# Performance work log

Measured on AMD Instinct MI355X. Metric: run time of the kernel, lower is better.

The kernel has to match this reference:

```python
import jax, jax.numpy as jnp
import numpy as np

N_NODES = 50000
N_REL = 8
N_EDGES = 100000
IN_SIZE = 128
OUT_SIZE = 128


def setup_inputs() -> dict:
    key = jax.random.key(0)
    k1, k2, k3, k4, k5 = jax.random.split(key, 5)
    inp = jax.random.normal(k1, (N_NODES, IN_SIZE), dtype=jnp.float32)
    src = jax.random.randint(k2, (N_REL, N_EDGES), 0, N_NODES, dtype=jnp.int32)
    dst = jax.random.randint(k3, (N_REL, N_EDGES), 0, N_NODES, dtype=jnp.int32)
    vals = jax.random.uniform(k4, (N_REL, N_EDGES), dtype=jnp.float32)
    weights = jax.random.normal(k5, (N_REL, IN_SIZE, OUT_SIZE), dtype=jnp.float32) * (1.0 / np.sqrt(IN_SIZE))
    return {"inp": inp, "src": src, "dst": dst, "vals": vals, "weights": weights}


def reference(inp, src, dst, vals, weights):
    # Per-relation sparse adj @ inp:  agg[r] = A_r @ inp, A_r given as COO edges.
    n_nodes = inp.shape[0]

    def rel_agg(s, d, v):
        msgs = v[:, None] * inp[s]                      # [E, in]
        return jax.ops.segment_sum(msgs, d, num_segments=n_nodes)  # [N, in]

    agg = jax.vmap(rel_agg)(src, dst, vals)             # [R, N, in]
    # concat along features then block-stacked weight matmul == per-relation
    # matmul summed over relations: out = sum_r agg[r] @ W[r]
    out = jnp.einsum('rni,rio->no', agg, weights)       # [N, out]
    return out
```

## Files before the change

kernel.cpp:

```cpp
#include <hip/hip_runtime.h>


constexpr int IN  = 128;
constexpr int OUT = 128;
constexpr int LDK = 136;
constexpr int NPB = 64;
constexpr int LDKB = 136;
constexpr int CAPMAX = 256;
constexpr int NBINS_MAX = 1024;
constexpr int EPB = 1024;

typedef __attribute__((ext_vector_type(8))) short bf16x8;
typedef __attribute__((ext_vector_type(4))) float f32x4;

__device__ inline unsigned short f2bf(float f) {
    unsigned int u = __float_as_uint(f);
    u += 0x7fffu + ((u >> 16) & 1u);
    return (unsigned short)(u >> 16);
}
__device__ inline float bflo(unsigned int u) { return __uint_as_float(u << 16); }
__device__ inline float bfhi(unsigned int u) { return __uint_as_float(u & 0xffff0000u); }
__device__ inline unsigned int pack2bf(float a, float b) {
    return (unsigned)f2bf(a) | ((unsigned)f2bf(b) << 16);
}
__device__ inline unsigned int cvtpk_bf16(float a, float b) {
    unsigned int r;
    asm("v_cvt_pk_bf16_f32 %0, %1, %2" : "=v"(r) : "v"(a), "v"(b));
    return r;
}

__global__ __launch_bounds__(256) void conv_inp_kernel(
    const float* __restrict__ x, unsigned short* __restrict__ y, int n8)
{
    const int i = blockIdx.x * 256 + threadIdx.x;
    if (i >= n8) return;
    const float4 a = ((const float4*)x)[i * 2];
    const float4 b = ((const float4*)x)[i * 2 + 1];
    uint4 o;
    o.x = pack2bf(a.x, a.y);
    o.y = pack2bf(a.z, a.w);
    o.z = pack2bf(b.x, b.y);
    o.w = pack2bf(b.z, b.w);
    ((uint4*)y)[i] = o;
}

__global__ __launch_bounds__(256) void conv_w_kernel(
    const float* __restrict__ w, unsigned short* __restrict__ wt, int total)
{
    const int t = blockIdx.x * 256 + threadIdx.x;
    if (t >= total) return;
    const int r = t >> 14, rem = t & 16383;
    const int n = rem >> 7, k = rem & 127;
    wt[t] = f2bf(w[(r << 14) + (k << 7) + n]);
}

__global__ __launch_bounds__(256) void prep_kernel(
    const int* __restrict__ src, const int* __restrict__ dst,
    const float* __restrict__ vals, int* __restrict__ bin_cnt,
    int2* __restrict__ binned, int4* __restrict__ spill,
    int* __restrict__ spill_cnt,
    int n_edges, int n_nodes, int nbins, int cap, int spill_max,
    int fgx, int nF,
    const float* __restrict__ x, unsigned short* __restrict__ y, int n8, int nbI,
    const float* __restrict__ w, unsigned short* __restrict__ wtb, int wtot)
{
    __shared__ int hist[NBINS_MAX];
    __shared__ int gbase[NBINS_MAX];

    const int bid = blockIdx.x;
    const int tid = threadIdx.x;

    if (bid >= nF) {
        const int cb = bid - nF;
        if (cb < nbI) {
            const int i = cb * 256 + tid;
            if (i >= n8) return;
            const float4 a = ((const float4*)x)[i * 2];
            const float4 b = ((const float4*)x)[i * 2 + 1];
            uint4 o;
            o.x = pack2bf(a.x, a.y);
            o.y = pack2bf(a.z, a.w);
            o.z = pack2bf(b.x, b.y);
            o.w = pack2bf(b.z, b.w);
            ((uint4*)y)[i] = o;
        } else {
            const int t = (cb - nbI) * 256 + tid;
            if (t >= wtot) return;
            const int r = t >> 14, rem = t & 16383;
            const int n = rem >> 7, k = rem & 127;
            wtb[t] = f2bf(w[(r << 14) + (k << 7) + n]);
        }
        return;
    }

    const int rel = bid / fgx;
    const int e0 = (bid - rel * fgx) * EPB;
    const size_t base_e = (size_t)rel * n_edges;

    for (int b = tid; b < nbins; b += 256) hist[b] = 0;
    __syncthreads();

    #pragma unroll
    for (int j = 0; j < EPB / 256; ++j) {
        const int e = e0 + j * 256 + tid;
        if (e < n_edges) atomicAdd(&hist[dst[base_e + e] >> 6], 1);
    }
    __syncthreads();

    for (int b = tid; b < nbins; b += 256) {
        const int c = hist[b];
        gbase[b] = c ? atomicAdd(&bin_cnt[rel * nbins + b], c) : 0;
        hist[b] = 0;
    }
    __syncthreads();

    #pragma unroll
    for (int j = 0; j < EPB / 256; ++j) {
        const int e = e0 + j * 256 + tid;
        if (e >= n_edges) continue;
        const int d = dst[base_e + e];
        const int s = src[base_e + e];
        const float v = vals[base_e + e];
        const int b = d >> 6;
        const int lp = atomicAdd(&hist[b], 1);
        const int pos = gbase[b] + lp;
        if (pos < cap) {
            binned[(size_t)(rel * nbins + b) * cap + pos] =
                make_int2(((d & 63) << 19) | s, __float_as_int(v));
        } else {
            const int sp = atomicAdd(spill_cnt, 1);
            if (sp < spill_max)
                spill[sp] = make_int4(d, (rel << 19) | s, __float_as_int(v), 0);
        }
    }
}

__global__ __launch_bounds__(256, 4) void bin_gemm_kernel(
    const unsigned short* __restrict__ inpb,
    const unsigned short* __restrict__ wt,
    const int2* __restrict__ binned, const int* __restrict__ bin_cnt,
    float* __restrict__ out, int n_nodes, int nbins, int cap, int n_rel)
{
    __shared__ unsigned short Ab[NPB * LDKB];
    __shared__ int2 sorted[CAPMAX];
    __shared__ int lcnt[NPB];
    __shared__ int loff[NPB + 1];
    __shared__ int lcur[NPB];
    __shared__ int relcnt[8];

    const int bin = blockIdx.x;
    const int tid = threadIdx.x;
    const int wave = tid >> 6, lane = tid & 63;
    const int m = lane & 15, q = lane >> 4;

    if (tid < n_rel) {
        int c = bin_cnt[tid * nbins + bin];
        relcnt[tid] = c > cap ? cap : c;
    }
    if (tid < NPB) { lcnt[tid] = 0; lcur[tid] = 0; }
    __syncthreads();

    int2 ecur = make_int2((NPB - 1) << 19, 0);
    if (tid < relcnt[0])
        ecur = binned[(size_t)bin * cap + tid];

    f32x4 acc[4][2];
    #pragma unroll
    for (int mt = 0; mt < 4; ++mt) {
        acc[mt][0] = (f32x4){0.f, 0.f, 0.f, 0.f};
        acc[mt][1] = (f32x4){0.f, 0.f, 0.f, 0.f};
    }

    for (int r = 0; r < n_rel; ++r) {
        const int cnt = relcnt[r];

        const unsigned short* wtr = wt + ((size_t)r * OUT + wave * 32) * IN;
        bf16x8 bfrag[2][4];
        #pragma unroll
        for (int nt = 0; nt < 2; ++nt)
            #pragma unroll
            for (int ks = 0; ks < 4; ++ks)
                bfrag[nt][ks] = *(const bf16x8*)(
                    wtr + (size_t)(nt * 16 + m) * IN + ks * 32 + q * 8);

        {
            uint4* A4 = (uint4*)Ab;
            #pragma unroll
            for (int j = 0; j < (NPB * LDKB / 8 + 255) / 256; ++j) {
                const int idx = j * 256 + tid;
                if (idx < NPB * LDKB / 8)
                    A4[idx] = make_uint4(0u, 0u, 0u, 0u);
            }
        }
        if (tid < cnt) atomicAdd(&lcnt[(ecur.x >> 19) & (NPB - 1)], 1);
        __syncthreads();

        if (tid < NPB) {
            const int v = lcnt[tid];
            int incl = v;
            #pragma unroll
            for (int off = 1; off < NPB; off <<= 1) {
                const int t = __shfl_up(incl, off, NPB);
                if (tid >= off) incl += t;
            }
            loff[tid] = incl - v;
            if (tid == NPB - 1) loff[NPB] = incl;
        }
        __syncthreads();

        if (tid < cnt) {
            const int g = (ecur.x >> 19) & (NPB - 1);
            const int pos = atomicAdd(&lcur[g], 1);
            sorted[loff[g] + pos] = ecur;
        }
        if (tid < NPB) lcnt[tid] = 0;
        __syncthreads();

        int2 enext = make_int2((NPB - 1) << 19, 0);
        if (r + 1 < n_rel && tid < relcnt[r + 1])
            enext = binned[(size_t)((r + 1) * nbins + bin) * cap + tid];

        {
            const int g0 = wave * 16;
            const int gend = g0 + 15;
            const int start = loff[g0];
            const int end = loff[g0 + 16];
            int cur = g0;
            float a0 = 0.f, a1 = 0.f;
            for (int i = start; i < end; i += 8) {
                int2 e[8]; unsigned int u[8];
                #pragma unroll
                for (int k = 0; k < 8; ++k) {
                    const int idx = i + k;
                    e[k] = (idx < end) ? sorted[idx]
                                       : make_int2(gend << 19, 0);
                }
                #pragma unroll
                for (int k = 0; k < 8; ++k)
                    u[k] = ((const unsigned int*)(
                        inpb + (size_t)(e[k].x & 0x7ffff) * IN))[lane];
                #pragma unroll
                for (int k = 0; k < 8; ++k) {
                    const int ln = (e[k].x >> 19) & 63;
                    if (ln != cur) {
                        *(unsigned int*)&Ab[cur * LDKB + lane * 2] =
                            cvtpk_bf16(a0, a1);
                        a0 = 0.f; a1 = 0.f; cur = ln;
                    }
                    const float v = __int_as_float(e[k].y);
                    a0 += v * bflo(u[k]); a1 += v * bfhi(u[k]);
                }
            }
            *(unsigned int*)&Ab[cur * LDKB + lane * 2] = cvtpk_bf16(a0, a1);
        }
        if (tid < NPB) lcur[tid] = 0;
        __syncthreads();

        #pragma unroll
        for (int ks = 0; ks < 4; ++ks) {
            bf16x8 a[4];
            #pragma unroll
            for (int mt = 0; mt < 4; ++mt)
                a[mt] = *(const bf16x8*)&Ab[(mt * 16 + m) * LDKB
                                            + ks * 32 + q * 8];
            #pragma unroll
            for (int mt = 0; mt < 4; ++mt) {
                acc[mt][0] = __builtin_amdgcn_mfma_f32_16x16x32_bf16(
                    a[mt], bfrag[0][ks], acc[mt][0], 0, 0, 0);
                acc[mt][1] = __builtin_amdgcn_mfma_f32_16x16x32_bf16(
                    a[mt], bfrag[1][ks], acc[mt][1], 0, 0, 0);
            }
        }
        ecur = enext;
        __syncthreads();
    }

    const int row0 = bin * NPB;
    #pragma unroll
    for (int mt = 0; mt < 4; ++mt) {
        #pragma unroll
        for (int rg = 0; rg < 4; ++rg) {
            const int row = row0 + mt * 16 + q * 4 + rg;
            if (row < n_nodes) {
                float* op = out + (size_t)row * OUT + wave * 32 + m;
                op[0]  = acc[mt][0][rg];
                op[16] = acc[mt][1][rg];
            }
        }
    }
}

__global__ __launch_bounds__(256) void spill_w_kernel(
    const unsigned short* __restrict__ inpb,
    const unsigned short* __restrict__ wt,
    const int4* __restrict__ spill, const int* __restrict__ spill_cnt,
    float* __restrict__ out, int spill_max)
{
    int n = *spill_cnt;
    if (n > spill_max) n = spill_max;
    const int w = (blockIdx.x * 256 + threadIdx.x) >> 6;
    const int lane = threadIdx.x & 63;
    const int nw = gridDim.x * 4;
    for (int i = w; i < n; i += nw) {
        const int4 s = spill[i];
        const int d = s.x;
        const int rel = s.y >> 19, srcrow = s.y & 0x7ffff;
        const float v = __int_as_float(s.z);
        const unsigned short* irow = inpb + (size_t)srcrow * IN;
        #pragma unroll
        for (int cc = 0; cc < 2; ++cc) {
            const int col = lane * 2 + cc;
            const unsigned short* wrow = wt + ((size_t)rel * OUT + col) * IN;
            float acc = 0.f;
            for (int k8 = 0; k8 < IN; k8 += 8) {
                const uint4 iw = *(const uint4*)(irow + k8);
                const uint4 ww = *(const uint4*)(wrow + k8);
                acc += bflo(iw.x)*bflo(ww.x) + bfhi(iw.x)*bfhi(ww.x)
                     + bflo(iw.y)*bflo(ww.y) + bfhi(iw.y)*bfhi(ww.y)
                     + bflo(iw.z)*bflo(ww.z) + bfhi(iw.z)*bfhi(ww.z)
                     + bflo(iw.w)*bflo(ww.w) + bfhi(iw.w)*bfhi(ww.w);
            }
            __hip_atomic_fetch_add(out + (size_t)d * OUT + col, v * acc,
                                   __ATOMIC_RELAXED, __HIP_MEMORY_SCOPE_AGENT);
        }
    }
}

__global__ __launch_bounds__(256) void mfma_gemm(
    const unsigned short* __restrict__ inpb,
    const unsigned short* __restrict__ wt,
    unsigned short* __restrict__ h, int rel_base, int n_nodes)
{
    __shared__ unsigned short As[128 * LDK];

    const int rel = rel_base + blockIdx.y;
    const int row0 = blockIdx.x * 128;
    const int tid = threadIdx.x;
    const int wave = tid >> 6, lane = tid & 63;
    const int m = lane & 15, q = lane >> 4;

    {
        const int r = tid >> 1;
        const int half = (tid & 1) * 64;
        const int grow = row0 + r;
        const uint4* gp = (const uint4*)(inpb + (size_t)grow * IN + half);
        uint4* lp = (uint4*)&As[r * LDK + half];
        #pragma unroll
        for (int i = 0; i < 8; ++i) {
            uint4 v = make_uint4(0u, 0u, 0u, 0u);
            if (grow < n_nodes) v = gp[i];
            lp[i] = v;
        }
    }

    bf16x8 bfrag[2][4];
    {
        const unsigned short* wtr = wt + ((size_t)rel * OUT + wave * 32) * IN;
        #pragma unroll
        for (int nt = 0; nt < 2; ++nt)
            #pragma unroll
            for (int ks = 0; ks < 4; ++ks)
                bfrag[nt][ks] = *(const bf16x8*)(
                    wtr + (size_t)(nt * 16 + m) * IN + ks * 32 + q * 8);
    }

    __syncthreads();

    f32x4 acc[8][2];
    #pragma unroll
    for (int mt = 0; mt < 8; ++mt)
        #pragma unroll
        for (int nt = 0; nt < 2; ++nt)
            acc[mt][nt] = (f32x4){0.f, 0.f, 0.f, 0.f};

    #pragma unroll
    for (int ks = 0; ks < 4; ++ks) {
        bf16x8 a[8];
        #pragma unroll
        for (int mt = 0; mt < 8; ++mt)
            a[mt] = *(const bf16x8*)&As[(mt * 16 + m) * LDK + ks * 32 + q * 8];
        #pragma unroll
        for (int mt = 0; mt < 8; ++mt) {
            acc[mt][0] = __builtin_amdgcn_mfma_f32_16x16x32_bf16(
                a[mt], bfrag[0][ks], acc[mt][0], 0, 0, 0);
            acc[mt][1] = __builtin_amdgcn_mfma_f32_16x16x32_bf16(
                a[mt], bfrag[1][ks], acc[mt][1], 0, 0, 0);
        }
    }

    unsigned short* hrel = h + (size_t)blockIdx.y * n_nodes * OUT;
    #pragma unroll
    for (int mt = 0; mt < 8; ++mt) {
        #pragma unroll
        for (int rg = 0; rg < 4; ++rg) {
            const int row = row0 + mt * 16 + q * 4 + rg;
            if (row < n_nodes) {
                unsigned short* hp = hrel + (size_t)row * OUT + wave * 32 + m;
                hp[0]  = f2bf(acc[mt][0][rg]);
                hp[16] = f2bf(acc[mt][1][rg]);
            }
        }
    }
}

__global__ __launch_bounds__(256) void fill_kernel(
    const int* __restrict__ src, const int* __restrict__ dst,
    const float* __restrict__ vals, int* __restrict__ counts,
    int2* __restrict__ bucket, int4* __restrict__ spill,
    int* __restrict__ spill_cnt, int n_edges, int n_nodes,
    int cap, int spill_max)
{
    const int e = blockIdx.x * 256 + threadIdx.x;
    if (e >= n_edges) return;
    const size_t g = (size_t)blockIdx.y * n_edges + e;
    const int d = dst[g];
    const int enc = blockIdx.y * n_nodes + src[g];
    const int pos = atomicAdd(&counts[d], 1);
    if (pos < cap) {
        bucket[(size_t)d * cap + pos] = make_int2(enc, __float_as_int(vals[g]));
    } else {
        const int sp = atomicAdd(spill_cnt, 1);
        if (sp < spill_max)
            spill[sp] = make_int4(d, enc, __float_as_int(vals[g]), 0);
    }
}

__global__ __launch_bounds__(256) void gather_kernel(
    const unsigned short* __restrict__ h, const int2* __restrict__ bucket,
    const int* __restrict__ counts, float* __restrict__ out,
    int n_nodes, int cap, int accum)
{
    const int node = blockIdx.x * 8 + (threadIdx.x >> 5);
    const int lane = threadIdx.x & 31;
    if (node >= n_nodes) return;
    int cnt = counts[node];
    if (cnt > cap) cnt = cap;
    const int2* __restrict__ b = bucket + (size_t)node * cap;
    float4* __restrict__ op = (float4*)(out + (size_t)node * OUT);

    float4 acc = accum ? op[lane] : make_float4(0.f, 0.f, 0.f, 0.f);
    int j = 0;
    for (; j + 4 <= cnt; j += 4) {
        const int2 r0 = b[j], r1 = b[j + 1], r2 = b[j + 2], r3 = b[j + 3];
        const uint2 h0 = ((const uint2*)(h + (size_t)r0.x * OUT))[lane];
        const uint2 h1 = ((const uint2*)(h + (size_t)r1.x * OUT))[lane];
        const uint2 h2 = ((const uint2*)(h + (size_t)r2.x * OUT))[lane];
        const uint2 h3 = ((const uint2*)(h + (size_t)r3.x * OUT))[lane];
        const float v0 = __int_as_float(r0.y), v1 = __int_as_float(r1.y);
        const float v2 = __int_as_float(r2.y), v3 = __int_as_float(r3.y);
        acc.x += v0*bflo(h0.x) + v1*bflo(h1.x) + v2*bflo(h2.x) + v3*bflo(h3.x);
        acc.y += v0*bfhi(h0.x) + v1*bfhi(h1.x) + v2*bfhi(h2.x) + v3*bfhi(h3.x);
        acc.z += v0*bflo(h0.y) + v1*bflo(h1.y) + v2*bflo(h2.y) + v3*bflo(h3.y);
        acc.w += v0*bfhi(h0.y) + v1*bfhi(h1.y) + v2*bfhi(h2.y) + v3*bfhi(h3.y);
    }
    for (; j < cnt; ++j) {
        const int2 r0 = b[j];
        const float v = __int_as_float(r0.y);
        const uint2 hv = ((const uint2*)(h + (size_t)r0.x * OUT))[lane];
        acc.x += v * bflo(hv.x); acc.y += v * bfhi(hv.x);
        acc.z += v * bflo(hv.y); acc.w += v * bfhi(hv.y);
    }
    op[lane] = acc;
}

__global__ __launch_bounds__(256) void spill_kernel(
    const unsigned short* __restrict__ h, const int4* __restrict__ spill,
    const int* __restrict__ spill_cnt, float* __restrict__ out, int spill_max)
{
    int n = *spill_cnt;
    if (n > spill_max) n = spill_max;
    const int w = (blockIdx.x * 256 + threadIdx.x) >> 6;
    const int lane = threadIdx.x & 63;
    const int nw = gridDim.x * 4;
    for (int i = w; i < n; i += nw) {
        const int4 s = spill[i];
        const float v = __int_as_float(s.z);
        const unsigned int u = ((const unsigned int*)(h + (size_t)s.y * OUT))[lane];
        float* __restrict__ orow = out + (size_t)s.x * OUT;
        __hip_atomic_fetch_add(orow + lane * 2,     v * bflo(u),
                               __ATOMIC_RELAXED, __HIP_MEMORY_SCOPE_AGENT);
        __hip_atomic_fetch_add(orow + lane * 2 + 1, v * bfhi(u),
                               __ATOMIC_RELAXED, __HIP_MEMORY_SCOPE_AGENT);
    }
}

__global__ __launch_bounds__(256) void scatter_kernel(
    const unsigned short* __restrict__ h, const int* __restrict__ src,
    const int* __restrict__ dst, const float* __restrict__ vals,
    float* __restrict__ out, int n_edges)
{
    const int e = blockIdx.x * 8 + (threadIdx.x >> 5);
    if (e >= n_edges) return;
    const int lane = threadIdx.x & 31;
    const int s = src[e];
    const int d = dst[e];
    const float v = vals[e];
    const unsigned int* __restrict__ hrow =
        (const unsigned int*)(h + (size_t)s * OUT);
    float* __restrict__ orow = out + (size_t)d * OUT;
    #pragma unroll
    for (int kk = 0; kk < 2; ++kk) {
        const int jj = lane + kk * 32;
        const unsigned int u = hrow[jj];
        __hip_atomic_fetch_add(orow + jj * 2,     v * bflo(u),
                               __ATOMIC_RELAXED, __HIP_MEMORY_SCOPE_AGENT);
        __hip_atomic_fetch_add(orow + jj * 2 + 1, v * bfhi(u),
                               __ATOMIC_RELAXED, __HIP_MEMORY_SCOPE_AGENT);
    }
}

extern "C" void kernel_launch(void* const* d_in, const int* in_sizes, int n_in,
                              void* d_out, int out_size, void* d_ws, size_t ws_size,
                              hipStream_t stream) {
    const float* inp     = (const float*)d_in[0];
    const int*   src     = (const int*)  d_in[1];
    const int*   dst     = (const int*)  d_in[2];
    const float* vals    = (const float*)d_in[3];
    const float* weights = (const float*)d_in[4];
    float* out = (float*)d_out;

    const int n_nodes = in_sizes[0] / IN;
    const int n_rel   = in_sizes[4] / (IN * OUT);
    const int n_edges = in_sizes[1] / n_rel;

    auto align_up = [](size_t x) { return (x + 255) & ~(size_t)255; };
    const int SPILL_MAX = 65536;
    const size_t sz_inpb   = align_up((size_t)n_nodes * IN * 2);
    const size_t sz_wt     = align_up((size_t)n_rel * IN * OUT * 2);
    const size_t sz_spill  = align_up((size_t)SPILL_MAX * 16);

    const int conv_n8 = n_nodes * IN / 8;
    const int wt_tot  = n_rel * IN * OUT;
    const int gemm_gx = (n_nodes + 127) / 128;
    const int gath_gx = (n_nodes + 7) / 8;
    const int fill_gx = (n_edges + 255) / 256;
    const int nbins   = (n_nodes + NPB - 1) / NPB;

    if (n_rel <= 8 && n_nodes < (1 << 19) && nbins <= NBINS_MAX) {
        const size_t ncells  = (size_t)n_rel * nbins;
        const size_t sz_bcnt = align_up((ncells + 1) * 4);
        int cap = 0;
        const int caps[] = {256, 192, 128};
        for (int c : caps) {
            const size_t sz_binned = align_up(ncells * c * 8);
            if (sz_inpb + sz_wt + sz_bcnt + sz_spill + sz_binned <= ws_size) {
                cap = c; break;
            }
        }
        if (cap > 0) {
            const size_t sz_binned = align_up(ncells * cap * 8);
            char* p = (char*)d_ws;
            unsigned short* inpb = (unsigned short*)p;  p += sz_inpb;
            unsigned short* wtb  = (unsigned short*)p;  p += sz_wt;
            int*   bin_cnt = (int*)p;   p += sz_bcnt;
            int4*  spill   = (int4*)p;  p += sz_spill;
            int2*  binned  = (int2*)p;  p += sz_binned;
            int*   spill_cnt = bin_cnt + ncells;

            const int nbI = (conv_n8 + 255) / 256;
            const int nbW = (wt_tot + 255) / 256;
            const int fgx = (n_edges + EPB - 1) / EPB;
            const int nF  = fgx * n_rel;

            hipMemsetAsync(bin_cnt, 0, (ncells + 1) * 4, stream);
            prep_kernel<<<nF + nbI + nbW, 256, 0, stream>>>(
                src, dst, vals, bin_cnt, binned, spill, spill_cnt,
                n_edges, n_nodes, nbins, cap, SPILL_MAX, fgx, nF,
                inp, inpb, conv_n8, nbI, weights, wtb, wt_tot);
            bin_gemm_kernel<<<nbins, 256, 0, stream>>>(
                inpb, wtb, binned, bin_cnt, out, n_nodes, nbins, cap, n_rel);
            spill_w_kernel<<<128, 256, 0, stream>>>(
                inpb, wtb, spill, spill_cnt, out, SPILL_MAX);
            return;
        }
    }

    const size_t sz_counts = align_up((size_t)(n_nodes + 1) * 4);
    const size_t fixed = sz_inpb + sz_wt + sz_counts + sz_spill;

    {
        const size_t sz_h = (size_t)n_rel * n_nodes * OUT * 2;
        int cap = 0;
        const int caps[] = {64, 48, 32, 24, 20};
        for (int c : caps) {
            if (fixed + sz_h + align_up((size_t)n_nodes * c * 8) <= ws_size) {
                cap = c; break;
            }
        }
        if (cap > 0) {
            char* p = (char*)d_ws;
            unsigned short* inpb = (unsigned short*)p;  p += sz_inpb;
            unsigned short* wtb  = (unsigned short*)p;  p += sz_wt;
            int*   counts = (int*)p;    p += sz_counts;
            int4*  spill  = (int4*)p;   p += sz_spill;
            unsigned short* h = (unsigned short*)p;     p += sz_h;
            int2*  bucket = (int2*)p;
            int*   spill_cnt = counts + n_nodes;

            conv_inp_kernel<<<(conv_n8 + 255) / 256, 256, 0, stream>>>(
                inp, inpb, conv_n8);
            conv_w_kernel<<<(wt_tot + 255) / 256, 256, 0, stream>>>(
                weights, wtb, wt_tot);
            hipMemsetAsync(counts, 0, (size_t)(n_nodes + 1) * 4, stream);
            dim3 fg(fill_gx, n_rel);
            fill_kernel<<<fg, 256, 0, stream>>>(src, dst, vals, counts, bucket,
                                                spill, spill_cnt, n_edges,
                                                n_nodes, cap, SPILL_MAX);
            dim3 gg(gemm_gx, n_rel);
            mfma_gemm<<<gg, 256, 0, stream>>>(inpb, wtb, h, 0, n_nodes);
            gather_kernel<<<gath_gx, 256, 0, stream>>>(h, bucket, counts, out,
                                                       n_nodes, cap, 0);
            spill_kernel<<<128, 256, 0, stream>>>(h, spill, spill_cnt, out,
                                                  SPILL_MAX);
            return;
        }
    }

    {
        char* p = (char*)d_ws;
        unsigned short* inpb = (unsigned short*)p;  p += sz_inpb;
        unsigned short* wtb  = (unsigned short*)p;  p += sz_wt;
        unsigned short* h = (unsigned short*)p;

        conv_inp_kernel<<<(conv_n8 + 255) / 256, 256, 0, stream>>>(
            inp, inpb, conv_n8);
        conv_w_kernel<<<(wt_tot + 255) / 256, 256, 0, stream>>>(
            weights, wtb, wt_tot);
        hipMemsetAsync(out, 0, (size_t)n_nodes * OUT * 4, stream);
        const int sgx = (n_edges + 7) / 8;
        for (int r = 0; r < n_rel; ++r) {
            const size_t eoff = (size_t)r * n_edges;
            dim3 gg(gemm_gx, 1);
            mfma_gemm<<<gg, 256, 0, stream>>>(inpb, wtb, h, r, n_nodes);
            scatter_kernel<<<sgx, 256, 0, stream>>>(h, src + eoff, dst + eoff,
                                                    vals + eoff, out, n_edges);
        }
    }
}
```

Baseline: 184.9 us.

## Fuse binning prep and bin GEMM into one cooperative persistent kernel

Merges the prep kernel (bf16 conversion of inputs and weights, edge binning) and the per-bin GEMM kernel into a single cooperative launch. Producer blocks pull tasks from an atomic queue and signal completion per relation; consumer bin blocks spin-wait on per-relation counters so each relation's GEMM can start as soon as its binning finishes. This aims to remove a kernel boundary and overlap binning with aggregation. The cost is spin-wait overhead, host-side occupancy and attribute queries on every call, and dependence on cooperative launch support, with the old two-kernel path kept as a fallback.

```diff
diff --git a/kernel.cpp b/kernel.cpp
--- a/kernel.cpp
+++ b/kernel.cpp
@@ -9,6 +9,7 @@
 constexpr int CAPMAX = 256;
 constexpr int NBINS_MAX = 1024;
 constexpr int EPB = 1024;
+constexpr int CCH = 2048;
 
 typedef __attribute__((ext_vector_type(8))) short bf16x8;
 typedef __attribute__((ext_vector_type(4))) float f32x4;
@@ -29,140 +30,127 @@
     return r;
 }
 
-__global__ __launch_bounds__(256) void conv_inp_kernel(
-    const float* __restrict__ x, unsigned short* __restrict__ y, int n8)
-{
-    const int i = blockIdx.x * 256 + threadIdx.x;
-    if (i >= n8) return;
-    const float4 a = ((const float4*)x)[i * 2];
-    const float4 b = ((const float4*)x)[i * 2 + 1];
-    uint4 o;
-    o.x = pack2bf(a.x, a.y);
-    o.y = pack2bf(a.z, a.w);
-    o.z = pack2bf(b.x, b.y);
-    o.w = pack2bf(b.z, b.w);
-    ((uint4*)y)[i] = o;
-}
-
-__global__ __launch_bounds__(256) void conv_w_kernel(
-    const float* __restrict__ w, unsigned short* __restrict__ wt, int total)
-{
-    const int t = blockIdx.x * 256 + threadIdx.x;
-    if (t >= total) return;
-    const int r = t >> 14, rem = t & 16383;
-    const int n = rem >> 7, k = rem & 127;
-    wt[t] = f2bf(w[(r << 14) + (k << 7) + n]);
-}
-
-__global__ __launch_bounds__(256) void prep_kernel(
+__global__ __launch_bounds__(256, 4) void fused_kernel(
+    const float* __restrict__ inp, const float* __restrict__ w,
     const int* __restrict__ src, const int* __restrict__ dst,
-    const float* __restrict__ vals, int* __restrict__ bin_cnt,
-    int2* __restrict__ binned, int4* __restrict__ spill,
-    int* __restrict__ spill_cnt,
+    const float* __restrict__ vals,
+    unsigned short* __restrict__ inpb, unsigned short* __restrict__ wtb,
+    int* __restrict__ bin_cnt, int2* __restrict__ binned,
+    int4* __restrict__ spill, int* __restrict__ spill_cnt,
+    int* __restrict__ ctrl, float* __restrict__ out,
     int n_edges, int n_nodes, int nbins, int cap, int spill_max,
-    int fgx, int nF,
-    const float* __restrict__ x, unsigned short* __restrict__ y, int n8, int nbI,
-    const float* __restrict__ w, unsigned short* __restrict__ wtb, int wtot)
-{
-    __shared__ int hist[NBINS_MAX];
-    __shared__ int gbase[NBINS_MAX];
-
-    const int bid = blockIdx.x;
-    const int tid = threadIdx.x;
-
-    if (bid >= nF) {
-        const int cb = bid - nF;
-        if (cb < nbI) {
-            const int i = cb * 256 + tid;
-            if (i >= n8) return;
-            const float4 a = ((const float4*)x)[i * 2];
-            const float4 b = ((const float4*)x)[i * 2 + 1];
-            uint4 o;
-            o.x = pack2bf(a.x, a.y);
-            o.y = pack2bf(a.z, a.w);
-            o.z = pack2bf(b.x, b.y);
-            o.w = pack2bf(b.z, b.w);
-            ((uint4*)y)[i] = o;
-        } else {
-            const int t = (cb - nbI) * 256 + tid;
-            if (t >= wtot) return;
-            const int r = t >> 14, rem = t & 16383;
-            const int n = rem >> 7, k = rem & 127;
-            wtb[t] = f2bf(w[(r << 14) + (k << 7) + n]);
-        }
-        return;
-    }
-
-    const int rel = bid / fgx;
-    const int e0 = (bid - rel * fgx) * EPB;
-    const size_t base_e = (size_t)rel * n_edges;
-
-    for (int b = tid; b < nbins; b += 256) hist[b] = 0;
-    __syncthreads();
-
-    #pragma unroll
-    for (int j = 0; j < EPB / 256; ++j) {
-        const int e = e0 + j * 256 + tid;
-        if (e < n_edges) atomicAdd(&hist[dst[base_e + e] >> 6], 1);
-    }
-    __syncthreads();
-
-    for (int b = tid; b < nbins; b += 256) {
-        const int c = hist[b];
-        gbase[b] = c ? atomicAdd(&bin_cnt[rel * nbins + b], c) : 0;
-        hist[b] = 0;
-    }
-    __syncthreads();
-
-    #pragma unroll
-    for (int j = 0; j < EPB / 256; ++j) {
-        const int e = e0 + j * 256 + tid;
-        if (e >= n_edges) continue;
-        const int d = dst[base_e + e];
-        const int s = src[base_e + e];
-        const float v = vals[base_e + e];
-        const int b = d >> 6;
-        const int lp = atomicAdd(&hist[b], 1);
-        const int pos = gbase[b] + lp;
-        if (pos < cap) {
-            binned[(size_t)(rel * nbins + b) * cap + pos] =
-                make_int2(((d & 63) << 19) | s, __float_as_int(v));
-        } else {
-            const int sp = atomicAdd(spill_cnt, 1);
-            if (sp < spill_max)
-                spill[sp] = make_int4(d, (rel << 19) | s, __float_as_int(v), 0);
-        }
-    }
-}
-
-__global__ __launch_bounds__(256, 4) void bin_gemm_kernel(
-    const unsigned short* __restrict__ inpb,
-    const unsigned short* __restrict__ wt,
-    const int2* __restrict__ binned, const int* __restrict__ bin_cnt,
-    float* __restrict__ out, int n_nodes, int nbins, int cap, int n_rel)
+    int fgx, int ntW, int ntI, int nprod, int n_rel)
 {
     __shared__ unsigned short Ab[NPB * LDKB];
     __shared__ int2 sorted[CAPMAX];
     __shared__ int lcnt[NPB];
     __shared__ int loff[NPB + 1];
     __shared__ int lcur[NPB];
-    __shared__ int relcnt[8];
-
-    const int bin = blockIdx.x;
+    __shared__ int tbcast;
+
+    const int bid = blockIdx.x;
     const int tid = threadIdx.x;
+
+    if (bid < nprod) {
+        int* hist  = (int*)Ab;
+        int* gbase = hist + NBINS_MAX;
+        const int wt_tot  = n_rel * IN * OUT;
+        const int conv_n8 = n_nodes * IN / 8;
+        const int ntasks  = ntW + ntI + n_rel * fgx;
+
+        for (;;) {
+            if (tid == 0)
+                tbcast = __hip_atomic_fetch_add(&ctrl[0], 1, __ATOMIC_RELAXED,
+                                                __HIP_MEMORY_SCOPE_AGENT);
+            __syncthreads();
+            const int t = tbcast;
+            if (t >= ntasks) return;
+
+            int* done;
+            if (t < ntW) {
+                const int base = t * CCH + tid * 8;
+                #pragma unroll
+                for (int i = 0; i < 8; ++i) {
+                    const int e = base + i;
+                    if (e < wt_tot) {
+                        const int r = e >> 14, rem = e & 16383;
+                        const int n = rem >> 7, k = rem & 127;
+                        wtb[e] = f2bf(w[(r << 14) + (k << 7) + n]);
+                    }
+                }
+                done = &ctrl[1];
+            } else if (t < ntW + ntI) {
+                const int c0 = (t - ntW) * CCH;
+                #pragma unroll
+                for (int j = 0; j < 8; ++j) {
+                    const int i = c0 + j * 256 + tid;
+                    if (i < conv_n8) {
+                        const float4 a = ((const float4*)inp)[i * 2];
+                        const float4 b = ((const float4*)inp)[i * 2 + 1];
+                        uint4 o;
+                        o.x = pack2bf(a.x, a.y);
+                        o.y = pack2bf(a.z, a.w);
+                        o.z = pack2bf(b.x, b.y);
+                        o.w = pack2bf(b.z, b.w);
+                        ((uint4*)inpb)[i] = o;
+                    }
+                }
+                done = &ctrl[1];
+            } else {
+                const int f = t - ntW - ntI;
+                const int rel = f / fgx;
+                const int e0 = (f - rel * fgx) * EPB;
+                const size_t base_e = (size_t)rel * n_edges;
+
+                for (int b = tid; b < nbins; b += 256) hist[b] = 0;
+                __syncthreads();
+                #pragma unroll
+                for (int j = 0; j < EPB / 256; ++j) {
+                    const int e = e0 + j * 256 + tid;
+                    if (e < n_edges)
+                        atomicAdd(&hist[dst[base_e + e] >> 6], 1);
+                }
+                __syncthreads();
+                for (int b = tid; b < nbins; b += 256) {
+                    const int c = hist[b];
+                    gbase[b] = c ? atomicAdd(&bin_cnt[rel * nbins + b], c) : 0;
+                    hist[b] = 0;
+                }
+                __syncthreads();
+                #pragma unroll
+                for (int j = 0; j < EPB / 256; ++j) {
+                    const int e = e0 + j * 256 + tid;
+                    if (e >= n_edges) continue;
+                    const int d = dst[base_e + e];
+                    const int s = src[base_e + e];
+                    const float v = vals[base_e + e];
+                    const int b = d >> 6;
+                    const int lp = atomicAdd(&hist[b], 1);
+                    const int pos = gbase[b] + lp;
+                    if (pos < cap) {
+                        binned[(size_t)(rel * nbins + b) * cap + pos] =
+                            make_int2(((d & 63) << 19) | s, __float_as_int(v));
+                    } else {
+                        const int sp = atomicAdd(spill_cnt, 1);
+                        if (sp < spill_max)
+                            spill[sp] = make_int4(d, (rel << 19) | s,
+                                                  __float_as_int(v), 0);
+                    }
+                }
+                done = &ctrl[2 + rel];
+            }
+            __syncthreads();
+            if (tid == 0)
+                __hip_atomic_fetch_add(done, 1, __ATOMIC_RELEASE,
+                                       __HIP_MEMORY_SCOPE_AGENT);
+        }
+    }
+
+    const int bin = bid - nprod;
     const int wave = tid >> 6, lane = tid & 63;
     const int m = lane & 15, q = lane >> 4;
 
-    if (tid < n_rel) {
-        int c = bin_cnt[tid * nbins + bin];
-        relcnt[tid] = c > cap ? cap : c;
-    }
     if (tid < NPB) { lcnt[tid] = 0; lcur[tid] = 0; }
-    __syncthreads();
-
-    int2 ecur = make_int2((NPB - 1) << 19, 0);
-    if (tid < relcnt[0])
-        ecur = binned[(size_t)bin * cap + tid];
 
     f32x4 acc[4][2];
     #pragma unroll
@@ -172,9 +160,27 @@
     }
 
     for (int r = 0; r < n_rel; ++r) {
-        const int cnt = relcnt[r];
-
-        const unsigned short* wtr = wt + ((size_t)r * OUT + wave * 32) * IN;
+        if (tid == 0) {
+            if (r == 0) {
+                while (__hip_atomic_load(&ctrl[1], __ATOMIC_RELAXED,
+                                         __HIP_MEMORY_SCOPE_AGENT) < ntW + ntI)
+                    __builtin_amdgcn_s_sleep(8);
+            }
+            while (__hip_atomic_load(&ctrl[2 + r], __ATOMIC_RELAXED,
+                                     __HIP_MEMORY_SCOPE_AGENT) < fgx)
+                __builtin_amdgcn_s_sleep(8);
+            (void)__hip_atomic_load(&ctrl[2 + r], __ATOMIC_ACQUIRE,
+                                    __HIP_MEMORY_SCOPE_AGENT);
+        }
+        __syncthreads();
+
+        int cnt = bin_cnt[r * nbins + bin];
+        if (cnt > cap) cnt = cap;
+        int2 ecur = make_int2((NPB - 1) << 19, 0);
+        if (tid < cnt)
+            ecur = binned[(size_t)(r * nbins + bin) * cap + tid];
+
+        const unsigned short* wtr = wtb + ((size_t)r * OUT + wave * 32) * IN;
         bf16x8 bfrag[2][4];
         #pragma unroll
         for (int nt = 0; nt < 2; ++nt)
@@ -215,10 +221,6 @@
         }
         if (tid < NPB) lcnt[tid] = 0;
         __syncthreads();
-
-        int2 enext = make_int2((NPB - 1) << 19, 0);
-        if (r + 1 < n_rel && tid < relcnt[r + 1])
-            enext = binned[(size_t)((r + 1) * nbins + bin) * cap + tid];
 
         {
             const int g0 = wave * 16;
@@ -271,6 +273,237 @@
                     a[mt], bfrag[1][ks], acc[mt][1], 0, 0, 0);
             }
         }
+    }
+
+    const int row0 = bin * NPB;
+    #pragma unroll
+    for (int mt = 0; mt < 4; ++mt) {
+        #pragma unroll
+        for (int rg = 0; rg < 4; ++rg) {
+            const int row = row0 + mt * 16 + q * 4 + rg;
+            if (row < n_nodes) {
+                float* op = out + (size_t)row * OUT + wave * 32 + m;
+                op[0]  = acc[mt][0][rg];
+                op[16] = acc[mt][1][rg];
+            }
+        }
+    }
+}
+
+__global__ __launch_bounds__(256) void prep_kernel(
+    const int* __restrict__ src, const int* __restrict__ dst,
+    const float* __restrict__ vals, int* __restrict__ bin_cnt,
+    int2* __restrict__ binned, int4* __restrict__ spill,
+    int* __restrict__ spill_cnt,
+    int n_edges, int n_nodes, int nbins, int cap, int spill_max,
+    int fgx, int nF,
+    const float* __restrict__ x, unsigned short* __restrict__ y, int n8, int nbI,
+    const float* __restrict__ w, unsigned short* __restrict__ wtb, int wtot)
+{
+    __shared__ int hist[NBINS_MAX];
+    __shared__ int gbase[NBINS_MAX];
+
+    const int bid = blockIdx.x;
+    const int tid = threadIdx.x;
+
+    if (bid >= nF) {
+        const int cb = bid - nF;
+        if (cb < nbI) {
+            const int i = cb * 256 + tid;
+            if (i >= n8) return;
+            const float4 a = ((const float4*)x)[i * 2];
+            const float4 b = ((const float4*)x)[i * 2 + 1];
+            uint4 o;
+            o.x = pack2bf(a.x, a.y);
+            o.y = pack2bf(a.z, a.w);
+            o.z = pack2bf(b.x, b.y);
+            o.w = pack2bf(b.z, b.w);
+            ((uint4*)y)[i] = o;
+        } else {
+            const int t = (cb - nbI) * 256 + tid;
+            if (t >= wtot) return;
+            const int r = t >> 14, rem = t & 16383;
+            const int n = rem >> 7, k = rem & 127;
+            wtb[t] = f2bf(w[(r << 14) + (k << 7) + n]);
+        }
+        return;
+    }
+
+    const int rel = bid / fgx;
+    const int e0 = (bid - rel * fgx) * EPB;
+    const size_t base_e = (size_t)rel * n_edges;
+
+    for (int b = tid; b < nbins; b += 256) hist[b] = 0;
+    __syncthreads();
+    #pragma unroll
+    for (int j = 0; j < EPB / 256; ++j) {
+        const int e = e0 + j * 256 + tid;
+        if (e < n_edges) atomicAdd(&hist[dst[base_e + e] >> 6], 1);
+    }
+    __syncthreads();
+    for (int b = tid; b < nbins; b += 256) {
+        const int c = hist[b];
+        gbase[b] = c ? atomicAdd(&bin_cnt[rel * nbins + b], c) : 0;
+        hist[b] = 0;
+    }
+    __syncthreads();
+    #pragma unroll
+    for (int j = 0; j < EPB / 256; ++j) {
+        const int e = e0 + j * 256 + tid;
+        if (e >= n_edges) continue;
+        const int d = dst[base_e + e];
+        const int s = src[base_e + e];
+        const float v = vals[base_e + e];
+        const int b = d >> 6;
+        const int lp = atomicAdd(&hist[b], 1);
+        const int pos = gbase[b] + lp;
+        if (pos < cap) {
+            binned[(size_t)(rel * nbins + b) * cap + pos] =
+                make_int2(((d & 63) << 19) | s, __float_as_int(v));
+        } else {
+            const int sp = atomicAdd(spill_cnt, 1);
+            if (sp < spill_max)
+                spill[sp] = make_int4(d, (rel << 19) | s, __float_as_int(v), 0);
+        }
+    }
+}
+
+__global__ __launch_bounds__(256, 4) void bin_gemm_kernel(
+    const unsigned short* __restrict__ inpb,
+    const unsigned short* __restrict__ wt,
+    const int2* __restrict__ binned, const int* __restrict__ bin_cnt,
+    float* __restrict__ out, int n_nodes, int nbins, int cap, int n_rel)
+{
+    __shared__ unsigned short Ab[NPB * LDKB];
+    __shared__ int2 sorted[CAPMAX];
+    __shared__ int lcnt[NPB];
+    __shared__ int loff[NPB + 1];
+    __shared__ int lcur[NPB];
+    __shared__ int relcnt[8];
+
+    const int bin = blockIdx.x;
+    const int tid = threadIdx.x;
+    const int wave = tid >> 6, lane = tid & 63;
+    const int m = lane & 15, q = lane >> 4;
+
+    if (tid < n_rel) {
+        int c = bin_cnt[tid * nbins + bin];
+        relcnt[tid] = c > cap ? cap : c;
+    }
+    if (tid < NPB) { lcnt[tid] = 0; lcur[tid] = 0; }
+    __syncthreads();
+
+    int2 ecur = make_int2((NPB - 1) << 19, 0);
+    if (tid < relcnt[0])
+        ecur = binned[(size_t)bin * cap + tid];
+
+    f32x4 acc[4][2];
+    #pragma unroll
+    for (int mt = 0; mt < 4; ++mt) {
+        acc[mt][0] = (f32x4){0.f, 0.f, 0.f, 0.f};
+        acc[mt][1] = (f32x4){0.f, 0.f, 0.f, 0.f};
+    }
+
+    for (int r = 0; r < n_rel; ++r) {
+        const int cnt = relcnt[r];
+
+        const unsigned short* wtr = wt + ((size_t)r * OUT + wave * 32) * IN;
+        bf16x8 bfrag[2][4];
+        #pragma unroll
+        for (int nt = 0; nt < 2; ++nt)
+            #pragma unroll
+            for (int ks = 0; ks < 4; ++ks)
+                bfrag[nt][ks] = *(const bf16x8*)(
+                    wtr + (size_t)(nt * 16 + m) * IN + ks * 32 + q * 8);
+
+        {
+            uint4* A4 = (uint4*)Ab;
+            #pragma unroll
+            for (int j = 0; j < (NPB * LDKB / 8 + 255) / 256; ++j) {
+                const int idx = j * 256 + tid;
+                if (idx < NPB * LDKB / 8)
+                    A4[idx] = make_uint4(0u, 0u, 0u, 0u);
+            }
+        }
+        if (tid < cnt) atomicAdd(&lcnt[(ecur.x >> 19) & (NPB - 1)], 1);
+        __syncthreads();
+
+        if (tid < NPB) {
+            const int v = lcnt[tid];
+            int incl = v;
+            #pragma unroll
+            for (int off = 1; off < NPB; off <<= 1) {
+                const int t = __shfl_up(incl, off, NPB);
+                if (tid >= off) incl += t;
+            }
+            loff[tid] = incl - v;
+            if (tid == NPB - 1) loff[NPB] = incl;
+        }
+        __syncthreads();
+
+        if (tid < cnt) {
+            const int g = (ecur.x >> 19) & (NPB - 1);
+            const int pos = atomicAdd(&lcur[g], 1);
+            sorted[loff[g] + pos] = ecur;
+        }
+        if (tid < NPB) lcnt[tid] = 0;
+        __syncthreads();
+
+        int2 enext = make_int2((NPB - 1) << 19, 0);
+        if (r + 1 < n_rel && tid < relcnt[r + 1])
+            enext = binned[(size_t)((r + 1) * nbins + bin) * cap + tid];
+
+        {
+            const int g0 = wave * 16;
+            const int gend = g0 + 15;
+            const int start = loff[g0];
+            const int end = loff[g0 + 16];
+            int cur = g0;
+            float a0 = 0.f, a1 = 0.f;
+            for (int i = start; i < end; i += 8) {
+                int2 e[8]; unsigned int u[8];
+                #pragma unroll
+                for (int k = 0; k < 8; ++k) {
+                    const int idx = i + k;
+                    e[k] = (idx < end) ? sorted[idx]
+                                       : make_int2(gend << 19, 0);
+                }
+                #pragma unroll
+                for (int k = 0; k < 8; ++k)
+                    u[k] = ((const unsigned int*)(
+                        inpb + (size_t)(e[k].x & 0x7ffff) * IN))[lane];
+                #pragma unroll
+                for (int k = 0; k < 8; ++k) {
+                    const int ln = (e[k].x >> 19) & 63;
+                    if (ln != cur) {
+                        *(unsigned int*)&Ab[cur * LDKB + lane * 2] =
+                            cvtpk_bf16(a0, a1);
+                        a0 = 0.f; a1 = 0.f; cur = ln;
+                    }
+                    const float v = __int_as_float(e[k].y);
+                    a0 += v * bflo(u[k]); a1 += v * bfhi(u[k]);
+                }
+            }
+            *(unsigned int*)&Ab[cur * LDKB + lane * 2] = cvtpk_bf16(a0, a1);
+        }
+        if (tid < NPB) lcur[tid] = 0;
+        __syncthreads();
+
+        #pragma unroll
+        for (int ks = 0; ks < 4; ++ks) {
+            bf16x8 a[4];
+            #pragma unroll
+            for (int mt = 0; mt < 4; ++mt)
+                a[mt] = *(const bf16x8*)&Ab[(mt * 16 + m) * LDKB
+                                            + ks * 32 + q * 8];
+            #pragma unroll
+            for (int mt = 0; mt < 4; ++mt) {
+                acc[mt][0] = __builtin_amdgcn_mfma_f32_16x16x32_bf16(
+                    a[mt], bfrag[0][ks], acc[mt][0], 0, 0, 0);
+                acc[mt][1] = __builtin_amdgcn_mfma_f32_16x16x32_bf16(
+                    a[mt], bfrag[1][ks], acc[mt][1], 0, 0, 0);
+            }
+        }
         ecur = enext;
         __syncthreads();
     }
@@ -324,6 +557,31 @@
                                    __ATOMIC_RELAXED, __HIP_MEMORY_SCOPE_AGENT);
         }
     }
+}
+
+__global__ __launch_bounds__(256) void conv_inp_kernel(
+    const float* __restrict__ x, unsigned short* __restrict__ y, int n8)
+{
+    const int i = blockIdx.x * 256 + threadIdx.x;
+    if (i >= n8) return;
+    const float4 a = ((const float4*)x)[i * 2];
+    const float4 b = ((const float4*)x)[i * 2 + 1];
+    uint4 o;
+    o.x = pack2bf(a.x, a.y);
+    o.y = pack2bf(a.z, a.w);
+    o.z = pack2bf(b.x, b.y);
+    o.w = pack2bf(b.z, b.w);
+    ((uint4*)y)[i] = o;
+}
+
+__global__ __launch_bounds__(256) void conv_w_kernel(
+    const float* __restrict__ w, unsigned short* __restrict__ wt, int total)
+{
+    const int t = blockIdx.x * 256 + threadIdx.x;
+    if (t >= total) return;
+    const int r = t >> 14, rem = t & 16383;
+    const int n = rem >> 7, k = rem & 127;
+    wt[t] = f2bf(w[(r << 14) + (k << 7) + n]);
 }
 
 __global__ __launch_bounds__(256) void mfma_gemm(
@@ -519,12 +777,12 @@
     const float* weights = (const float*)d_in[4];
     float* out = (float*)d_out;
 
-    const int n_nodes = in_sizes[0] / IN;
-    const int n_rel   = in_sizes[4] / (IN * OUT);
-    const int n_edges = in_sizes[1] / n_rel;
+    int n_edges = in_sizes[1] / (in_sizes[4] / (IN * OUT));
+    int n_nodes = in_sizes[0] / IN;
+    int n_rel   = in_sizes[4] / (IN * OUT);
 
     auto align_up = [](size_t x) { return (x + 255) & ~(size_t)255; };
-    const int SPILL_MAX = 65536;
+    int SPILL_MAX = 65536;
     const size_t sz_inpb   = align_up((size_t)n_nodes * IN * 2);
     const size_t sz_wt     = align_up((size_t)n_rel * IN * OUT * 2);
     const size_t sz_spill  = align_up((size_t)SPILL_MAX * 16);
@@ -534,11 +792,11 @@
     const int gemm_gx = (n_nodes + 127) / 128;
     const int gath_gx = (n_nodes + 7) / 8;
     const int fill_gx = (n_edges + 255) / 256;
-    const int nbins   = (n_nodes + NPB - 1) / NPB;
+    int nbins   = (n_nodes + NPB - 1) / NPB;
 
     if (n_rel <= 8 && n_nodes < (1 << 19) && nbins <= NBINS_MAX) {
         const size_t ncells  = (size_t)n_rel * nbins;
-        const size_t sz_bcnt = align_up((ncells + 1) * 4);
+        const size_t sz_bcnt = align_up((ncells + 17) * 4);
         int cap = 0;
         const int caps[] = {256, 192, 128};
         for (int c : caps) {
@@ -556,19 +814,53 @@
             int4*  spill   = (int4*)p;  p += sz_spill;
             int2*  binned  = (int2*)p;  p += sz_binned;
             int*   spill_cnt = bin_cnt + ncells;
-
-            const int nbI = (conv_n8 + 255) / 256;
-            const int nbW = (wt_tot + 255) / 256;
-            const int fgx = (n_edges + EPB - 1) / EPB;
-            const int nF  = fgx * n_rel;
-
-            hipMemsetAsync(bin_cnt, 0, (ncells + 1) * 4, stream);
-            prep_kernel<<<nF + nbI + nbW, 256, 0, stream>>>(
-                src, dst, vals, bin_cnt, binned, spill, spill_cnt,
-                n_edges, n_nodes, nbins, cap, SPILL_MAX, fgx, nF,
-                inp, inpb, conv_n8, nbI, weights, wtb, wt_tot);
-            bin_gemm_kernel<<<nbins, 256, 0, stream>>>(
-                inpb, wtb, binned, bin_cnt, out, n_nodes, nbins, cap, n_rel);
+            int*   ctrl      = bin_cnt + ncells + 1;
+
+            int fgx = (n_edges + EPB - 1) / EPB;
+            int ntW = (wt_tot + CCH - 1) / CCH;
+            int ntI = (conv_n8 + CCH - 1) / CCH;
+
+            hipMemsetAsync(bin_cnt, 0, (ncells + 17) * 4, stream);
+
+            bool launched = false;
+            int dev = 0;
+            hipGetDevice(&dev);
+            int coop = 0, ncu = 0;
+            hipDeviceGetAttribute(&coop, hipDeviceAttributeCooperativeLaunch, dev);
+            hipDeviceGetAttribute(&ncu, hipDeviceAttributeMultiprocessorCount, dev);
+            int occ = 0;
+            hipOccupancyMaxActiveBlocksPerMultiprocessor(&occ, fused_kernel, 256, 0);
+            const int maxco = occ * ncu;
+            if (coop && maxco >= nbins + 64) {
+                int nprod = maxco - nbins;
+                if (nprod > 512) nprod = 512;
+                void* args[] = {
+                    (void*)&inp, (void*)&weights, (void*)&src, (void*)&dst,
+                    (void*)&vals, (void*)&inpb, (void*)&wtb, (void*)&bin_cnt,
+                    (void*)&binned, (void*)&spill, (void*)&spill_cnt,
+                    (void*)&ctrl, (void*)&out,
+                    (void*)&n_edges, (void*)&n_nodes, (void*)&nbins,
+                    (void*)&cap, (void*)&SPILL_MAX, (void*)&fgx,
+                    (void*)&ntW, (void*)&ntI, (void*)&nprod, (void*)&n_rel };
+                hipError_t err = hipLaunchCooperativeKernel(
+                    fused_kernel, dim3(nbins + nprod), dim3(256),
+                    args, 0, stream);
+                if (err == hipSuccess) launched = true;
+            }
+
+            if (!launched) {
+                hipMemsetAsync(bin_cnt, 0, (ncells + 17) * 4, stream);
+                const int nbI = (conv_n8 + 255) / 256;
+                const int nbW = (wt_tot + 255) / 256;
+                const int nF  = fgx * n_rel;
+                prep_kernel<<<nF + nbI + nbW, 256, 0, stream>>>(
+                    src, dst, vals, bin_cnt, binned, spill, spill_cnt,
+                    n_edges, n_nodes, nbins, cap, SPILL_MAX, fgx, nF,
+                    inp, inpb, conv_n8, nbI, weights, wtb, wt_tot);
+                bin_gemm_kernel<<<nbins, 256, 0, stream>>>(
+                    inpb, wtb, binned, bin_cnt, out, n_nodes, nbins, cap,
+                    n_rel);
+            }
             spill_w_kernel<<<128, 256, 0, stream>>>(
                 inpb, wtb, spill, spill_cnt, out, SPILL_MAX);
             return;
```

Measured after the change: 189.1 us. 2.3% more time.
